# Kernel tuning notes

Measured on AMD Instinct MI355X. Metric: run time of the kernel, lower is better.

Reference implementation:

```python
import jax, jax.numpy as jnp
import numpy as np


def log_g(x):
    # log of g(x) where g(x) = x + 0.5 for x >= 0 else sigmoid(x)
    return jnp.where(x >= 0, jnp.log(jnp.where(x >= 0, x, 0.0) + 0.5), -jax.nn.softplus(-x))


def mingru_layer(x, h0, W, b):
    # x: (B,S,Din), h0: (B,1,H) positive, W: (2H,Din), b: (2H,)
    gh = jnp.einsum('bsd,ed->bse', x, W) + b
    gate, hidden = jnp.split(gh, 2, axis=-1)
    log_z = -jax.nn.softplus(-gate)        # log sigmoid(gate)
    log_coeffs = -jax.nn.softplus(gate)    # log (1 - sigmoid(gate))
    log_values = jnp.concatenate([jnp.log(h0), log_z + log_g(hidden)], axis=1)  # (B,S+1,H)
    a_star = jnp.pad(jnp.cumsum(log_coeffs, axis=1), ((0, 0), (1, 0), (0, 0)))  # (B,S+1,H)
    log_h = a_star + jax.lax.cumlogsumexp(log_values - a_star, axis=1)
    return jnp.exp(log_h)[:, 1:]  # (B,S,H)


def setup_inputs() -> dict:
    key = jax.random.key(0)
    ks = jax.random.split(key, 6)
    B, S, D, H = 8, 2048, 1024, 1024
    L = 2
    s = 0.02
    return {
        'x': jax.random.normal(ks[0], (B, S, D), jnp.float32),
        'h': jax.random.uniform(ks[1], (L, B, 1, H), jnp.float32, 0.05, 1.0),
        'w0': jax.random.normal(ks[2], (2 * H, D), jnp.float32) * s,
        'b0': jax.random.normal(ks[3], (2 * H,), jnp.float32) * s,
        'w1': jax.random.normal(ks[4], (2 * H, H), jnp.float32) * s,
        'b1': jax.random.normal(ks[5], (2 * H,), jnp.float32) * s,
    }


def reference(x, h, w0, b0, w1, b1):
    # layer 0 (residual, align = Identity since input_dims == hidden_dims)
    out0 = mingru_layer(x, h[0], w0, b0)
    h0_final = out0[:, -1:]
    inp = out0 + x
    # layer 1 (last layer: residual, no dropout after)
    out1 = mingru_layer(inp, h[1], w1, b1)
    h1_final = out1[:, -1:]
    out = out1 + inp
    h_final = jnp.stack([h0_final, h1_final])  # (L,B,1,H)
    return out, h_final
```

## Files before the change

kernel.cpp:

```cpp
#include <hip/hip_runtime.h>
#include <hip/hip_bf16.h>
#include <cstdint>
#include <cstddef>

#define GAS __attribute__((address_space(1)))
#define LAS __attribute__((address_space(3)))

typedef __attribute__((ext_vector_type(8))) __bf16 bf16x8;
typedef __attribute__((ext_vector_type(4))) float f32x4;

constexpr int kB = 8, kS = 2048, kK = 1024, kH = 1024;
constexpr int kM = kB * kS;
constexpr int kN2 = 2 * kH;
constexpr int BM = 128, BK = 32;
constexpr int NKT = kK / BK;
constexpr int kChunks = 16;

constexpr size_t kOffXb   = 0;
constexpr size_t kOffW0   = 33554432;
constexpr size_t kOffW1   = 37748736;
constexpr size_t kOffA    = 41943040;
constexpr size_t kOffG    = 75497472;
constexpr size_t kOffCA   = 109051904;
constexpr size_t kOffCV   = 109576192;
constexpr size_t kOffHst  = 110100480;
constexpr size_t kWsNeed  = 115343360;

__device__ __forceinline__ ushort f2bf(float f) {
    union { float f; uint32_t u; } v; v.f = f;
    uint32_t r = v.u + 0x7FFFu + ((v.u >> 16) & 1u);
    return (ushort)(r >> 16);
}
__device__ __forceinline__ float bf2f(ushort u) {
    union { uint32_t u; float f; } v; v.u = (uint32_t)u << 16;
    return v.f;
}

constexpr int QX = kM * kK / 4;
constexpr int QW = kN2 * kK / 4;
__global__ void cvt3_kernel(const float* __restrict__ x, const float* __restrict__ w0,
                            const float* __restrict__ w1,
                            ushort* __restrict__ xb, ushort* __restrict__ w0b,
                            ushort* __restrict__ w1b)
{
    int i = blockIdx.x * 256 + threadIdx.x;
    const float* s; ushort* d;
    if (i < QX)            { s = x  + (size_t)i * 4;            d = xb  + (size_t)i * 4; }
    else if (i < QX + QW)  { int k = i - QX;      s = w0 + (size_t)k * 4; d = w0b + (size_t)k * 4; }
    else                   { int k = i - QX - QW; s = w1 + (size_t)k * 4; d = w1b + (size_t)k * 4; }
    f32x4 v = *reinterpret_cast<const f32x4*>(s);
    ushort4 o;
    o.x = f2bf(v.x); o.y = f2bf(v.y); o.z = f2bf(v.z); o.w = f2bf(v.w);
    *reinterpret_cast<ushort4*>(d) = o;
}

__global__ __launch_bounds__(256, 2)
void gemm_scan_kernel(const ushort* __restrict__ A, const ushort* __restrict__ W,
                      const float* __restrict__ bias,
                      ushort* __restrict__ Apref, ushort* __restrict__ Vpref,
                      float* __restrict__ cA, float* __restrict__ cV)
{
    __shared__ ushort smem[37888];

    const int tid  = threadIdx.x;
    const int lane = tid & 63;
    const int wv   = tid >> 6;
    const int wm   = wv >> 1;
    const int wn   = wv & 1;

    const int bid = blockIdx.x;
    const int sid = (bid & 7) * 128 + (bid >> 3);
    const int tm  = sid >> 3;
    const int tn  = sid & 7;
    const int m0  = tm * BM;
    const int j0  = tn * 128;
    const int b   = tm >> 4;
    const int c   = tm & 15;

    f32x4 acc[4][8];
#pragma unroll
    for (int i = 0; i < 4; ++i)
#pragma unroll
        for (int j = 0; j < 8; ++j) acc[i][j] = (f32x4){0.f, 0.f, 0.f, 0.f};

    const int srow  = tid >> 2;
    const int sslot = (tid & 3) ^ ((tid >> 3) & 3);
    const int scol  = sslot * 8;
    const int tid16 = tid * 16;

    const ushort* ga0 = A + (size_t)(m0 + srow) * kK + scol;
    const ushort* gb0 = W + (size_t)(j0 + srow) * kK + scol;
    const ushort* gb1 = W + (size_t)(1024 + j0 + srow) * kK + scol;

    char* lds = (char*)smem;

    const int rslot = (lane >> 4) ^ ((lane >> 1) & 3);
    const int rb    = (lane & 15) * 64 + rslot * 16;
    const int aoff  = wm * 4096 + rb;
    const int boff  = 8192 + wn * 8192 + rb;

#define VMWAIT(N) asm volatile("s_waitcnt vmcnt(" #N ")" ::: "memory")

#define STG3A(S) do {                                                            \
    __builtin_amdgcn_global_load_lds((const GAS void*)(ga0),                     \
        (LAS void*)(lds + (S) * 24576 + tid16),          16, 0, 0);              \
    __builtin_amdgcn_global_load_lds((const GAS void*)(ga0 + 65536),             \
        (LAS void*)(lds + (S) * 24576 + 4096 + tid16),   16, 0, 0);              \
    __builtin_amdgcn_global_load_lds((const GAS void*)(gb0),                     \
        (LAS void*)(lds + (S) * 24576 + 8192 + tid16),   16, 0, 0);              \
  } while (0)

#define STG3B(S) do {                                                            \
    __builtin_amdgcn_global_load_lds((const GAS void*)(gb0 + 65536),             \
        (LAS void*)(lds + (S) * 24576 + 12288 + tid16),  16, 0, 0);              \
    __builtin_amdgcn_global_load_lds((const GAS void*)(gb1),                     \
        (LAS void*)(lds + (S) * 24576 + 16384 + tid16),  16, 0, 0);              \
    __builtin_amdgcn_global_load_lds((const GAS void*)(gb1 + 65536),             \
        (LAS void*)(lds + (S) * 24576 + 20480 + tid16),  16, 0, 0);              \
    ga0 += BK; gb0 += BK; gb1 += BK;                                             \
  } while (0)

#define TILE_GEN(BUF, SA, SB, EW) do {                                           \
    bf16x8 af_[4], bf_[4];                                                       \
    _Pragma("unroll")                                                            \
    for (int mf_ = 0; mf_ < 4; ++mf_)                                            \
        af_[mf_] = *reinterpret_cast<const bf16x8*>(                             \
            lds + (BUF) * 24576 + aoff + mf_ * 1024);                            \
    _Pragma("unroll")                                                            \
    for (int nf_ = 0; nf_ < 4; ++nf_)                                            \
        bf_[nf_] = *reinterpret_cast<const bf16x8*>(                             \
            lds + (BUF) * 24576 + boff + nf_ * 1024);                            \
    SA;                                                                          \
    __builtin_amdgcn_s_barrier();                                                \
    asm volatile("s_waitcnt lgkmcnt(0)" ::: "memory");                           \
    __builtin_amdgcn_sched_barrier(0);                                           \
    __builtin_amdgcn_s_setprio(1);                                               \
    _Pragma("unroll")                                                            \
    for (int mf_ = 0; mf_ < 4; ++mf_)                                            \
        _Pragma("unroll")                                                        \
        for (int nf_ = 0; nf_ < 4; ++nf_)                                        \
            acc[mf_][nf_] = __builtin_amdgcn_mfma_f32_16x16x32_bf16(             \
                af_[mf_], bf_[nf_], acc[mf_][nf_], 0, 0, 0);                     \
    __builtin_amdgcn_s_setprio(0);                                               \
    __builtin_amdgcn_s_barrier();                                                \
    _Pragma("unroll")                                                            \
    for (int nf_ = 0; nf_ < 4; ++nf_)                                            \
        bf_[nf_] = *reinterpret_cast<const bf16x8*>(                             \
            lds + (BUF) * 24576 + boff + (4 + nf_) * 1024);                      \
    SB;                                                                          \
    __builtin_amdgcn_s_barrier();                                                \
    asm volatile("s_waitcnt lgkmcnt(0)" ::: "memory");                           \
    __builtin_amdgcn_sched_barrier(0);                                           \
    __builtin_amdgcn_s_setprio(1);                                               \
    _Pragma("unroll")                                                            \
    for (int mf_ = 0; mf_ < 4; ++mf_)                                            \
        _Pragma("unroll")                                                        \
        for (int nf_ = 0; nf_ < 4; ++nf_)                                        \
            acc[mf_][4 + nf_] = __builtin_amdgcn_mfma_f32_16x16x32_bf16(         \
                af_[mf_], bf_[nf_], acc[mf_][4 + nf_], 0, 0, 0);                 \
    __builtin_amdgcn_s_setprio(0);                                               \
    EW;                                                                          \
    __builtin_amdgcn_s_barrier();                                                \
  } while (0)

#define TILE(BUF, SBUF) TILE_GEN(BUF, STG3A(SBUF), STG3B(SBUF), VMWAIT(6))
#define TAIL0(BUF)      TILE_GEN(BUF, (void)0, (void)0, VMWAIT(0))
#define TAIL1(BUF)      TILE_GEN(BUF, (void)0, (void)0, (void)0)

    STG3A(0); STG3B(0);
    STG3A(1); STG3B(1);
    VMWAIT(6);
    __builtin_amdgcn_s_barrier();

    for (int g = 0; g < 10; ++g) {
        TILE(0, 2);
        TILE(1, 0);
        TILE(2, 1);
    }
    TAIL0(0);
    TAIL1(1);

#undef TILE
#undef TAIL0
#undef TAIL1
#undef TILE_GEN
#undef STG3A
#undef STG3B
#undef VMWAIT

    ushort* a_lds = smem;
    ushort* g_lds = smem + 16896;
    f32x4*  sA4   = (f32x4*)(lds + 67584);
    f32x4*  sV4   = (f32x4*)(lds + 71680);

    {
        const bool isG = (wn == 0);
        ushort* tgt = isG ? a_lds : g_lds;
        float bn[8];
#pragma unroll
        for (int nf = 0; nf < 8; ++nf)
            bn[nf] = bias[(isG ? 0 : 1024) + j0 + nf * 16 + (lane & 15)];
#pragma unroll
        for (int mf = 0; mf < 4; ++mf) {
#pragma unroll
            for (int i = 0; i < 4; ++i) {
                const int m = wm * 64 + mf * 16 + (lane >> 4) * 4 + i;
#pragma unroll
                for (int nf = 0; nf < 8; ++nf) {
                    float val = acc[mf][nf][i] + bn[nf];
                    float r;
                    if (isG) r = 1.f / (1.f + __expf(val));
                    else     r = (val >= 0.f) ? val + 0.5f : 1.f / (1.f + __expf(-val));
                    tgt[m * 132 + nf * 16 + (lane & 15)] = f2bf(r);
                }
            }
        }
    }
    __syncthreads();

    {
        const int jq = tid & 31;
        const int sg = tid >> 5;
        f32x4 A1 = (f32x4){1.f, 1.f, 1.f, 1.f};
        f32x4 V1 = (f32x4){0.f, 0.f, 0.f, 0.f};
#pragma unroll 4
        for (int t = 0; t < 16; ++t) {
            const int s = sg * 16 + t;
            ushort4 au = *reinterpret_cast<const ushort4*>(a_lds + s * 132 + jq * 4);
            ushort4 gu = *reinterpret_cast<const ushort4*>(g_lds + s * 132 + jq * 4);
            f32x4 a = (f32x4){bf2f(au.x), bf2f(au.y), bf2f(au.z), bf2f(au.w)};
            f32x4 g = (f32x4){bf2f(gu.x), bf2f(gu.y), bf2f(gu.z), bf2f(gu.w)};
            V1 = a * V1 + (1.f - a) * g;
            A1 *= a;
        }
        sA4[sg * 32 + jq] = A1;
        sV4[sg * 32 + jq] = V1;
        __syncthreads();
        f32x4 Ar = (f32x4){1.f, 1.f, 1.f, 1.f};
        f32x4 Vr = (f32x4){0.f, 0.f, 0.f, 0.f};
        for (int k = 0; k < sg; ++k) {
            f32x4 Ak = sA4[k * 32 + jq], Vk = sV4[k * 32 + jq];
            Vr = Ak * Vr + Vk;
            Ar *= Ak;
        }
        ushort* ApG = Apref + (size_t)(m0 + sg * 16) * kH + j0 + jq * 4;
        ushort* VpG = Vpref + (size_t)(m0 + sg * 16) * kH + j0 + jq * 4;
#pragma unroll 4
        for (int t = 0; t < 16; ++t) {
            const int s = sg * 16 + t;
            ushort4 au = *reinterpret_cast<const ushort4*>(a_lds + s * 132 + jq * 4);
            ushort4 gu = *reinterpret_cast<const ushort4*>(g_lds + s * 132 + jq * 4);
            f32x4 a = (f32x4){bf2f(au.x), bf2f(au.y), bf2f(au.z), bf2f(au.w)};
            f32x4 g = (f32x4){bf2f(gu.x), bf2f(gu.y), bf2f(gu.z), bf2f(gu.w)};
            Vr = a * Vr + (1.f - a) * g;
            Ar *= a;
            ushort4 oa, ov;
            oa.x = f2bf(Ar.x); oa.y = f2bf(Ar.y); oa.z = f2bf(Ar.z); oa.w = f2bf(Ar.w);
            ov.x = f2bf(Vr.x); ov.y = f2bf(Vr.y); ov.z = f2bf(Vr.z); ov.w = f2bf(Vr.w);
            *reinterpret_cast<ushort4*>(ApG) = oa;
            *reinterpret_cast<ushort4*>(VpG) = ov;
            ApG += kH; VpG += kH;
        }
        if (sg == 7) {
            size_t o = ((size_t)(b * kChunks + c) << 10) + j0 + jq * 4;
            *reinterpret_cast<f32x4*>(cA + o) = Ar;
            *reinterpret_cast<f32x4*>(cV + o) = Vr;
        }
    }
}

__global__ void scan_chunks_kernel(const float* __restrict__ cA, const float* __restrict__ cV,
                                   const float* __restrict__ h0, float* __restrict__ hstart,
                                   float* __restrict__ hfin)
{
    int idx = blockIdx.x * 256 + threadIdx.x;
    int j = idx & 1023, bb = idx >> 10;
    float h = h0[(bb << 10) + j];
    for (int c = 0; c < kChunks; ++c) {
        int o = ((bb * kChunks + c) << 10) + j;
        hstart[o] = h;
        h = cA[o] * h + cV[o];
    }
    hfin[(bb << 10) + j] = h;
}

template<bool WRITE_F32>
__global__ void apply_kernel(const ushort* __restrict__ Ap, const ushort* __restrict__ Vp,
                             const float* __restrict__ hst, const ushort* __restrict__ res,
                             void* __restrict__ outp)
{
    size_t i = ((size_t)blockIdx.x * 256 + threadIdx.x) * 4;
    int m = (int)(i >> 10);
    int j = (int)(i & 1023);
    int bb = m >> 11, s = m & 2047, c = s >> 7;
    f32x4 hcs = *reinterpret_cast<const f32x4*>(hst + (((bb * kChunks + c) << 10) + j));
    ushort4 Au = *reinterpret_cast<const ushort4*>(Ap + i);
    ushort4 Vu = *reinterpret_cast<const ushort4*>(Vp + i);
    ushort4 Ru = *reinterpret_cast<const ushort4*>(res + i);
    f32x4 o;
    o.x = bf2f(Au.x) * hcs.x + bf2f(Vu.x) + bf2f(Ru.x);
    o.y = bf2f(Au.y) * hcs.y + bf2f(Vu.y) + bf2f(Ru.y);
    o.z = bf2f(Au.z) * hcs.z + bf2f(Vu.z) + bf2f(Ru.z);
    o.w = bf2f(Au.w) * hcs.w + bf2f(Vu.w) + bf2f(Ru.w);
    if (WRITE_F32) {
        *reinterpret_cast<f32x4*>((float*)outp + i) = o;
    } else {
        ushort4 ob;
        ob.x = f2bf(o.x); ob.y = f2bf(o.y); ob.z = f2bf(o.z); ob.w = f2bf(o.w);
        *reinterpret_cast<ushort4*>((ushort*)outp + i) = ob;
    }
}

extern "C" void kernel_launch(void* const* d_in, const int* in_sizes, int n_in,
                              void* d_out, int out_size, void* d_ws, size_t ws_size,
                              hipStream_t stream)
{
    const float* x  = (const float*)d_in[0];
    const float* h  = (const float*)d_in[1];
    const float* w0 = (const float*)d_in[2];
    const float* b0 = (const float*)d_in[3];
    const float* w1 = (const float*)d_in[4];
    const float* b1 = (const float*)d_in[5];
    float* out = (float*)d_out;
    char* ws = (char*)d_ws;

    if (ws_size < kWsNeed) return;

    ushort* xb   = (ushort*)(ws + kOffXb);
    ushort* inpb = (ushort*)(ws + kOffXb);
    ushort* w0b  = (ushort*)(ws + kOffW0);
    ushort* w1b  = (ushort*)(ws + kOffW1);
    ushort* Ap   = (ushort*)(ws + kOffA);
    ushort* Vp   = (ushort*)(ws + kOffG);
    float*  cA   = (float*)(ws + kOffCA);
    float*  cV   = (float*)(ws + kOffCV);
    float*  hst  = (float*)(ws + kOffHst);

    float* out_h = out + (size_t)kM * kH;

    cvt3_kernel<<<(QX + 2 * QW) / 256, 256, 0, stream>>>(x, w0, w1, xb, w0b, w1b);

    const int gemm_grid  = (kM / BM) * (kN2 / 256);
    const int apply_grid = kM * kH / 4 / 256;

    gemm_scan_kernel<<<gemm_grid, 256, 0, stream>>>(xb, w0b, b0, Ap, Vp, cA, cV);
    scan_chunks_kernel<<<32, 256, 0, stream>>>(cA, cV, h, hst, out_h);
    apply_kernel<false><<<apply_grid, 256, 0, stream>>>(Ap, Vp, hst, xb, inpb);

    gemm_scan_kernel<<<gemm_grid, 256, 0, stream>>>(inpb, w1b, b1, Ap, Vp, cA, cV);
    scan_chunks_kernel<<<32, 256, 0, stream>>>(cA, cV, h + (size_t)kB * kH, hst, out_h + (size_t)kB * kH);
    apply_kernel<true><<<apply_grid, 256, 0, stream>>>(Ap, Vp, hst, inpb, out);
}
```

Before: 269.1 us.

## Give each wave private LDS staging to drop block barriers in GEMM mainloop

Each wave now loads its own A and B slices into a private LDS region, so the main loop needs only vmcnt waits and no workgroup barriers. The cost being targeted is per-tile barrier synchronisation across the four waves. In exchange, A and B tiles are duplicated across waves, which doubles LDS use and global load traffic and forces occupancy down to one block per CU (launch bounds 1).

```diff
diff --git a/kernel.cpp b/kernel.cpp
--- a/kernel.cpp
+++ b/kernel.cpp
@@ -54,13 +54,13 @@
     *reinterpret_cast<ushort4*>(d) = o;
 }
 
-__global__ __launch_bounds__(256, 2)
+__global__ __launch_bounds__(256, 1)
 void gemm_scan_kernel(const ushort* __restrict__ A, const ushort* __restrict__ W,
                       const float* __restrict__ bias,
                       ushort* __restrict__ Apref, ushort* __restrict__ Vpref,
                       float* __restrict__ cA, float* __restrict__ cV)
 {
-    __shared__ ushort smem[37888];
+    __shared__ ushort smem[73728];
 
     const int tid  = threadIdx.x;
     const int lane = tid & 63;
@@ -83,110 +83,69 @@
 #pragma unroll
         for (int j = 0; j < 8; ++j) acc[i][j] = (f32x4){0.f, 0.f, 0.f, 0.f};
 
-    const int srow  = tid >> 2;
-    const int sslot = (tid & 3) ^ ((tid >> 3) & 3);
+    const int sslot = (lane & 3) ^ ((lane >> 3) & 3);
     const int scol  = sslot * 8;
-    const int tid16 = tid * 16;
-
-    const ushort* ga0 = A + (size_t)(m0 + srow) * kK + scol;
-    const ushort* gb0 = W + (size_t)(j0 + srow) * kK + scol;
-    const ushort* gb1 = W + (size_t)(1024 + j0 + srow) * kK + scol;
+
+    const ushort* gA = A + (size_t)(m0 + wm * 64 + (lane >> 2)) * kK + scol;
+    const ushort* gB = W + (size_t)((wn ? 1024 : 0) + j0 + (lane >> 2)) * kK + scol;
 
     char* lds = (char*)smem;
+    const int wbase = wv * 12288;
 
     const int rslot = (lane >> 4) ^ ((lane >> 1) & 3);
-    const int rb    = (lane & 15) * 64 + rslot * 16;
-    const int aoff  = wm * 4096 + rb;
-    const int boff  = 8192 + wn * 8192 + rb;
+    const int aoff  = wbase + (lane & 15) * 64 + rslot * 16;
+    const int boff  = aoff + 4096;
 
 #define VMWAIT(N) asm volatile("s_waitcnt vmcnt(" #N ")" ::: "memory")
 
-#define STG3A(S) do {                                                            \
-    __builtin_amdgcn_global_load_lds((const GAS void*)(ga0),                     \
-        (LAS void*)(lds + (S) * 24576 + tid16),          16, 0, 0);              \
-    __builtin_amdgcn_global_load_lds((const GAS void*)(ga0 + 65536),             \
-        (LAS void*)(lds + (S) * 24576 + 4096 + tid16),   16, 0, 0);              \
-    __builtin_amdgcn_global_load_lds((const GAS void*)(gb0),                     \
-        (LAS void*)(lds + (S) * 24576 + 8192 + tid16),   16, 0, 0);              \
+#define STAGE(BUF) do {                                                          \
+    _Pragma("unroll")                                                            \
+    for (int i_ = 0; i_ < 4; ++i_)                                               \
+        __builtin_amdgcn_global_load_lds((const GAS void*)(gA + (size_t)i_ * 16 * kK), \
+            (LAS void*)(lds + (BUF) * 49152 + wbase + i_ * 1024), 16, 0, 0);     \
+    _Pragma("unroll")                                                            \
+    for (int i_ = 0; i_ < 8; ++i_)                                               \
+        __builtin_amdgcn_global_load_lds((const GAS void*)(gB + (size_t)i_ * 16 * kK), \
+            (LAS void*)(lds + (BUF) * 49152 + wbase + 4096 + i_ * 1024), 16, 0, 0); \
+    gA += BK; gB += BK;                                                          \
   } while (0)
 
-#define STG3B(S) do {                                                            \
-    __builtin_amdgcn_global_load_lds((const GAS void*)(gb0 + 65536),             \
-        (LAS void*)(lds + (S) * 24576 + 12288 + tid16),  16, 0, 0);              \
-    __builtin_amdgcn_global_load_lds((const GAS void*)(gb1),                     \
-        (LAS void*)(lds + (S) * 24576 + 16384 + tid16),  16, 0, 0);              \
-    __builtin_amdgcn_global_load_lds((const GAS void*)(gb1 + 65536),             \
-        (LAS void*)(lds + (S) * 24576 + 20480 + tid16),  16, 0, 0);              \
-    ga0 += BK; gb0 += BK; gb1 += BK;                                             \
-  } while (0)
-
-#define TILE_GEN(BUF, SA, SB, EW) do {                                           \
-    bf16x8 af_[4], bf_[4];                                                       \
+#define COMPUTE(BUF) do {                                                        \
+    bf16x8 af_[4], bf_[8];                                                       \
     _Pragma("unroll")                                                            \
     for (int mf_ = 0; mf_ < 4; ++mf_)                                            \
         af_[mf_] = *reinterpret_cast<const bf16x8*>(                             \
-            lds + (BUF) * 24576 + aoff + mf_ * 1024);                            \
-    _Pragma("unroll")                                                            \
-    for (int nf_ = 0; nf_ < 4; ++nf_)                                            \
+            lds + (BUF) * 49152 + aoff + mf_ * 1024);                            \
+    _Pragma("unroll")                                                            \
+    for (int nf_ = 0; nf_ < 8; ++nf_)                                            \
         bf_[nf_] = *reinterpret_cast<const bf16x8*>(                             \
-            lds + (BUF) * 24576 + boff + nf_ * 1024);                            \
-    SA;                                                                          \
-    __builtin_amdgcn_s_barrier();                                                \
-    asm volatile("s_waitcnt lgkmcnt(0)" ::: "memory");                           \
-    __builtin_amdgcn_sched_barrier(0);                                           \
+            lds + (BUF) * 49152 + boff + nf_ * 1024);                            \
     __builtin_amdgcn_s_setprio(1);                                               \
     _Pragma("unroll")                                                            \
     for (int mf_ = 0; mf_ < 4; ++mf_)                                            \
         _Pragma("unroll")                                                        \
-        for (int nf_ = 0; nf_ < 4; ++nf_)                                        \
+        for (int nf_ = 0; nf_ < 8; ++nf_)                                        \
             acc[mf_][nf_] = __builtin_amdgcn_mfma_f32_16x16x32_bf16(             \
                 af_[mf_], bf_[nf_], acc[mf_][nf_], 0, 0, 0);                     \
     __builtin_amdgcn_s_setprio(0);                                               \
-    __builtin_amdgcn_s_barrier();                                                \
-    _Pragma("unroll")                                                            \
-    for (int nf_ = 0; nf_ < 4; ++nf_)                                            \
-        bf_[nf_] = *reinterpret_cast<const bf16x8*>(                             \
-            lds + (BUF) * 24576 + boff + (4 + nf_) * 1024);                      \
-    SB;                                                                          \
-    __builtin_amdgcn_s_barrier();                                                \
-    asm volatile("s_waitcnt lgkmcnt(0)" ::: "memory");                           \
-    __builtin_amdgcn_sched_barrier(0);                                           \
-    __builtin_amdgcn_s_setprio(1);                                               \
-    _Pragma("unroll")                                                            \
-    for (int mf_ = 0; mf_ < 4; ++mf_)                                            \
-        _Pragma("unroll")                                                        \
-        for (int nf_ = 0; nf_ < 4; ++nf_)                                        \
-            acc[mf_][4 + nf_] = __builtin_amdgcn_mfma_f32_16x16x32_bf16(         \
-                af_[mf_], bf_[nf_], acc[mf_][4 + nf_], 0, 0, 0);                 \
-    __builtin_amdgcn_s_setprio(0);                                               \
-    EW;                                                                          \
-    __builtin_amdgcn_s_barrier();                                                \
   } while (0)
 
-#define TILE(BUF, SBUF) TILE_GEN(BUF, STG3A(SBUF), STG3B(SBUF), VMWAIT(6))
-#define TAIL0(BUF)      TILE_GEN(BUF, (void)0, (void)0, VMWAIT(0))
-#define TAIL1(BUF)      TILE_GEN(BUF, (void)0, (void)0, (void)0)
-
-    STG3A(0); STG3B(0);
-    STG3A(1); STG3B(1);
-    VMWAIT(6);
-    __builtin_amdgcn_s_barrier();
+    STAGE(0);
+    STAGE(1);
 
     for (int g = 0; g < 10; ++g) {
-        TILE(0, 2);
-        TILE(1, 0);
-        TILE(2, 1);
-    }
-    TAIL0(0);
-    TAIL1(1);
-
-#undef TILE
-#undef TAIL0
-#undef TAIL1
-#undef TILE_GEN
-#undef STG3A
-#undef STG3B
+        STAGE(2); VMWAIT(24); COMPUTE(0);
+        STAGE(0); VMWAIT(24); COMPUTE(1);
+        STAGE(1); VMWAIT(24); COMPUTE(2);
+    }
+    VMWAIT(12); COMPUTE(0);
+    VMWAIT(0);  COMPUTE(1);
+
+#undef STAGE
+#undef COMPUTE
 #undef VMWAIT
+
+    __syncthreads();
 
     ushort* a_lds = smem;
     ushort* g_lds = smem + 16896;
```

New measurement: 369.7 us. +37.4%, slower.
